# Performance work log

Hardware: AMD Instinct MI355X
Metric: run time of the kernel (lower is better)

The kernel has to match this reference:

```python
import jax, jax.numpy as jnp
import numpy as np

B, S, IN_DIM, D_MODEL, H = 8, 1024, 512, 1024, 16
DEPTH = D_MODEL // H
LN_EPS = 1e-5


def setup_inputs() -> dict:
    key = jax.random.key(0)
    ks = jax.random.split(key, 10)
    def xavier(k, shape):
        fan_in, fan_out = shape[0], shape[1]
        lim = float(np.sqrt(6.0 / (fan_in + fan_out)))
        return jax.random.uniform(k, shape, jnp.float32, -lim, lim)
    return {
        "x": jax.random.normal(ks[0], (B, S, IN_DIM), jnp.float32),
        "mask": jax.random.randint(ks[1], (H, S, S), 0, 2, jnp.int32),
        "wq_w": xavier(ks[2], (IN_DIM, D_MODEL)),
        "wq_b": jnp.zeros((D_MODEL,), jnp.float32),
        "wk_w": xavier(ks[3], (IN_DIM, D_MODEL)),
        "wk_b": jnp.zeros((D_MODEL,), jnp.float32),
        "wv_w": xavier(ks[4], (IN_DIM, D_MODEL)),
        "wv_b": jnp.zeros((D_MODEL,), jnp.float32),
        "dense_w": xavier(ks[5], (D_MODEL, D_MODEL)),
        "dense_b": jnp.zeros((D_MODEL,), jnp.float32),
        "res_w": xavier(ks[6], (IN_DIM, D_MODEL)),  # residual_linear (no bias)
        "ln_g": 1.0 + 0.02 * jax.random.normal(ks[7], (D_MODEL,), jnp.float32),
        "ln_b": 0.02 * jax.random.normal(ks[8], (D_MODEL,), jnp.float32),
    }


def reference(x, mask, wq_w, wq_b, wk_w, wk_b, wv_w, wv_b,
              dense_w, dense_b, res_w, ln_g, ln_b):
    bs = x.shape[0]
    residual = x @ res_w  # [B,S,D_MODEL]
    # project and split heads -> [B,H,S,depth]
    def split(t):
        return t.reshape(bs, -1, H, DEPTH).transpose(0, 2, 1, 3)
    q = split(x @ wq_w + wq_b)
    k = split(x @ wk_w + wk_b)
    v = split(x @ wv_w + wv_b)
    scale = 1.0 / jnp.sqrt(jnp.asarray(DEPTH, x.dtype))
    attn = jnp.einsum("bhqd,bhkd->bhqk", q, k) * scale
    attn = jnp.where(mask[None] == 0, jnp.asarray(-1e9, attn.dtype), attn)
    attn = jax.nn.softmax(attn, axis=-1)  # dropout is identity in eval
    out = jnp.einsum("bhqk,bhkd->bhqd", attn, v)
    out = out.transpose(0, 2, 1, 3).reshape(bs, -1, D_MODEL)
    out = out @ dense_w + dense_b
    # residual + LayerNorm
    y = residual + out
    mu = jnp.mean(y, axis=-1, keepdims=True)
    var = jnp.mean(jnp.square(y - mu), axis=-1, keepdims=True)
    y = (y - mu) * jax.lax.rsqrt(var + LN_EPS)
    return y * ln_g + ln_b
```

## Files before the change

kernel.cpp:

```cpp
#include <hip/hip_runtime.h>
#include <stdint.h>

#define B_ 8
#define S_ 1024
#define IN_DIM 512
#define DM 1024
#define H_ 16
#define DEP 64

typedef __bf16 bf16;
typedef __attribute__((ext_vector_type(8))) __bf16 bf16x8;
typedef __attribute__((ext_vector_type(4))) __bf16 bf16x4;
typedef __attribute__((ext_vector_type(4))) float f32x4;

static __device__ __forceinline__ void gld_lds16(const void* g, void* l) {
    __builtin_amdgcn_global_load_lds(
        (const __attribute__((address_space(1))) uint32_t*)g,
        (__attribute__((address_space(3))) uint32_t*)l, 16, 0, 0);
}

__global__ void detect_kernel(const uint16_t* __restrict__ xraw, int* __restrict__ flag) {
    const int t = threadIdx.x;
    int sane = 0;
    #pragma unroll
    for (int j = 0; j < 8; j++) {
        const uint16_t u = xraw[t * 8 + j];
        const int e = (u >> 7) & 0xff;
        sane += ((u & 0x7fff) == 0 || (e >= 100 && e <= 140)) ? 1 : 0;
    }
    #pragma unroll
    for (int m = 1; m < 64; m <<= 1) sane += __shfl_xor(sane, m);
    if (t == 0) *flag = (sane >= 450) ? 1 : 0;
}

static __device__ __forceinline__ float ldin(const void* p, size_t i, int isb) {
    return isb ? (float)((const bf16*)p)[i] : ((const float*)p)[i];
}

__global__ __launch_bounds__(256) void transpose_kernel(
    const void* __restrict__ wq, const void* __restrict__ wk, const void* __restrict__ wv,
    const void* __restrict__ res, const void* __restrict__ dense,
    bf16* __restrict__ wqT, bf16* __restrict__ wkT, bf16* __restrict__ wvT,
    bf16* __restrict__ resT, bf16* __restrict__ denseT, const int* __restrict__ flag)
{
    const int isb = *flag;
    __shared__ bf16 tile[32][33];
    const int z = blockIdx.z;
    const void* src; bf16* dst; int kb, kd;
    if (z == 0)      { src = wq;    dst = wqT;    kb = 0;   kd = 512;  }
    else if (z == 1) { src = wk;    dst = wkT;    kb = 0;   kd = 512;  }
    else if (z == 2) { src = wv;    dst = wvT;    kb = 0;   kd = 512;  }
    else if (z == 3) { src = res;   dst = resT;   kb = 0;   kd = 512;  }
    else if (z == 4) { src = dense; dst = denseT; kb = 0;   kd = 1024; }
    else             { src = dense; dst = denseT; kb = 512; kd = 1024; }
    const int n0 = blockIdx.x * 32, k0 = blockIdx.y * 32;
    const int tx = threadIdx.x, ty = threadIdx.y;
    #pragma unroll
    for (int r = 0; r < 4; r++)
        tile[ty + r*8][tx] = (bf16)ldin(src, (size_t)(kb + k0 + ty + r*8) * DM + n0 + tx, isb);
    __syncthreads();
    #pragma unroll
    for (int r = 0; r < 4; r++)
        dst[(size_t)(n0 + ty + r*8) * kd + kb + k0 + tx] = tile[tx][ty + r*8];
}

__global__ __launch_bounds__(256) void xconv_kernel(
    const void* __restrict__ x, bf16* __restrict__ xc, const int* __restrict__ flag)
{
    const int isb = *flag;
    const size_t i = ((size_t)blockIdx.x * 256 + threadIdx.x) * 4;
    #pragma unroll
    for (int j = 0; j < 4; j++) xc[i + j] = (bf16)ldin(x, i + j, isb);
}

__global__ __launch_bounds__(256) void smallconv_kernel(
    const void* b0, const void* b1, const void* b2, const void* b3,
    const void* b4, const void* b5, bf16* __restrict__ out, const int* __restrict__ flag)
{
    const int isb = *flag;
    const void* srcs[6] = {b0, b1, b2, b3, b4, b5};
    const void* s = srcs[blockIdx.x];
    for (int i = threadIdx.x; i < 1024; i += 256)
        out[blockIdx.x * 1024 + i] = (bf16)ldin(s, i, isb);
}

__global__ __launch_bounds__(256) void maskpack_kernel(
    const int* __restrict__ mask, unsigned long long* __restrict__ mb)
{
    const int w = threadIdx.x >> 6, lane = threadIdx.x & 63;
    const int gw = blockIdx.x * 4 + w;
    for (int c = gw; c < 262144; c += 4096) {
        const int v = mask[(size_t)c * 64 + lane];
        const unsigned long long bits = __ballot(v != 0);
        if (lane == 0) mb[c] = bits;
    }
}

template<int KDIM>
static __device__ __forceinline__ void gemm_core(
    const bf16* __restrict__ A, const bf16* __restrict__ BT,
    int m0, int n0, bf16* Asm, bf16* Bsm, f32x4 acc[4][4])
{
    const int tid = threadIdx.x, l = tid & 63, w = tid >> 6;
    const int wm = w >> 1, wn = w & 1, quad = l >> 4, l15 = l & 15;
    #pragma unroll
    for (int i = 0; i < 4; i++)
        #pragma unroll
        for (int j = 0; j < 4; j++) acc[i][j] = f32x4{0.f, 0.f, 0.f, 0.f};

    for (int k0 = 0; k0 < KDIM; k0 += 32) {
        __syncthreads();
        #pragma unroll
        for (int qq = 0; qq < 2; qq++) {
            const int c = qq*256 + tid;
            const int row = c >> 2, ch = c & 3;
            gld_lds16(A  + (size_t)(m0 + row)*KDIM + k0 + ch*8, Asm + (qq*256 + w*64)*8);
            gld_lds16(BT + (size_t)(n0 + row)*KDIM + k0 + ch*8, Bsm + (qq*256 + w*64)*8);
        }
        __syncthreads();
        bf16x8 af[4], bfv[4];
        #pragma unroll
        for (int i = 0; i < 4; i++)
            af[i] = *(const bf16x8*)(Asm + (wm*64 + i*16 + l15)*32 + quad*8);
        #pragma unroll
        for (int j = 0; j < 4; j++)
            bfv[j] = *(const bf16x8*)(Bsm + (wn*64 + j*16 + l15)*32 + quad*8);
        #pragma unroll
        for (int i = 0; i < 4; i++)
            #pragma unroll
            for (int j = 0; j < 4; j++)
                acc[i][j] = __builtin_amdgcn_mfma_f32_16x16x32_bf16(af[i], bfv[j], acc[i][j], 0, 0, 0);
    }
}

#define EPI_P 132
__global__ __launch_bounds__(256) void proj_kernel(
    const bf16* __restrict__ x,
    const bf16* __restrict__ wqT, const bf16* __restrict__ wkT,
    const bf16* __restrict__ wvT, const bf16* __restrict__ resT,
    const bf16* __restrict__ small,
    bf16* __restrict__ Q, bf16* __restrict__ K, bf16* __restrict__ VtG, bf16* __restrict__ R)
{
    __shared__ alignas(16) char smem[17408];
    bf16* Asm = (bf16*)smem;
    bf16* Bsm = (bf16*)(smem + 8192);
    bf16* epi = (bf16*)smem;

    const int m0 = blockIdx.x * 128;
    const int ng = blockIdx.y * 128;
    const int sel = ng >> 10, n0 = ng & 1023;
    const bf16* BT; const bf16* bias = nullptr;
    if (sel == 0)      { BT = wqT; bias = small;        }
    else if (sel == 1) { BT = wkT; bias = small + 1024; }
    else if (sel == 2) { BT = wvT; bias = small + 2048; }
    else               { BT = resT; }

    f32x4 acc[4][4];
    gemm_core<IN_DIM>(x, BT, m0, n0, Asm, Bsm, acc);

    const int tid = threadIdx.x, l = tid & 63, w = tid >> 6;
    const int wm = w >> 1, wn = w & 1, quad = l >> 4, l15 = l & 15;

    if (sel == 2) {
        const int bb = m0 >> 10, srow0 = m0 & 1023;
        #pragma unroll
        for (int hf = 0; hf < 2; hf++) {
            __syncthreads();
            if (wn == hf) {
                #pragma unroll
                for (int j = 0; j < 4; j++) {
                    const int cl = j*16 + l15;
                    const float bv = (float)bias[n0 + hf*64 + cl];
                    #pragma unroll
                    for (int i = 0; i < 4; i++) {
                        const int rho = wm*64 + i*16 + quad*4;
                        #pragma unroll
                        for (int r = 0; r < 4; r++)
                            epi[cl*EPI_P + rho + r] = (bf16)(acc[i][j][r] + bv);
                    }
                }
            }
            __syncthreads();
            const int hh = (n0 >> 6) + hf;
            const int sc = tid & 15;
            #pragma unroll
            for (int pass = 0; pass < 4; pass++) {
                const int dl = (tid >> 4) + pass*16;
                bf16x8 v;
                #pragma unroll
                for (int k = 0; k < 8; k++) v[k] = epi[dl*EPI_P + sc*8 + k];
                *(bf16x8*)(VtG + ((size_t)(bb*16 + hh)*64 + dl)*S_ + srow0 + sc*8) = v;
            }
        }
        return;
    }

    #pragma unroll
    for (int j = 0; j < 4; j++) {
        const int col = n0 + wn*64 + j*16 + l15;
        const float bv = (sel < 3) ? (float)bias[col] : 0.f;
        #pragma unroll
        for (int i = 0; i < 4; i++) {
            const int rb = m0 + wm*64 + i*16 + quad*4;
            #pragma unroll
            for (int r = 0; r < 4; r++) {
                const float v = acc[i][j][r] + bv;
                if (sel == 0)      Q[(size_t)(rb + r)*DM + col] = (bf16)(v * 0.125f);
                else if (sel == 1) K[(size_t)(rb + r)*DM + col] = (bf16)v;
                else               R[(size_t)(rb + r)*DM + col] = (bf16)v;
            }
        }
    }
}

#define KP 68
__global__ __launch_bounds__(256) void attn_kernel(
    const bf16* __restrict__ Q, const bf16* __restrict__ K, const bf16* __restrict__ VtG,
    const unsigned long long* __restrict__ mb, bf16* __restrict__ AO)
{
    __shared__ alignas(16) bf16 Ksm[64*KP];
    __shared__ alignas(16) bf16 Vsm[64*KP];
    __shared__ alignas(16) bf16 Psm[4*16*40];

    const int tid = threadIdx.x, l = tid & 63, w = tid >> 6;
    const int quad = l >> 4, l15 = l & 15;
    const int b = blockIdx.y >> 4, h = blockIdx.y & 15;
    const int wrow = blockIdx.x*128 + w*32;
    const size_t rowbase = (size_t)b * S_;
    bf16* pp = Psm + w*640;

    bf16x8 qa[2][2];
    #pragma unroll
    for (int g = 0; g < 2; g++) {
        const bf16* qp = Q + (rowbase + wrow + g*16 + l15)*DM + h*DEP + quad*8;
        qa[g][0] = *(const bf16x8*)qp;
        qa[g][1] = *(const bf16x8*)(qp + 32);
    }
    const bf16* kgbase = K + rowbase*DM + h*DEP;
    const bf16* vgbase = VtG + (size_t)(b*16 + h)*64*S_;
    const unsigned long long* mrow[2][4];
    #pragma unroll
    for (int g = 0; g < 2; g++)
        #pragma unroll
        for (int r = 0; r < 4; r++)
            mrow[g][r] = mb + ((size_t)h*S_ + wrow + g*16 + quad*4 + r) * 16;

    f32x4 o[2][4];
    float lsum[2][4];
    #pragma unroll
    for (int g = 0; g < 2; g++)
        #pragma unroll
        for (int dt = 0; dt < 4; dt++) { o[g][dt] = f32x4{0.f,0.f,0.f,0.f}; lsum[g][dt] = 0.f; }

    const int srow = tid >> 3, sch = tid & 7;

    for (int kt = 0; kt < S_; kt += 64) {
        uint32_t mw[2][2][4];
        #pragma unroll
        for (int g = 0; g < 2; g++)
            #pragma unroll
            for (int r = 0; r < 4; r++) {
                const unsigned long long m = mrow[g][r][kt >> 6];
                mw[g][0][r] = (uint32_t)m;
                mw[g][1][r] = (uint32_t)(m >> 32);
            }
        const bf16x8 k0v = *(const bf16x8*)(kgbase + (size_t)(kt + srow)*DM + sch*8);
        const bf16x8 k1v = *(const bf16x8*)(kgbase + (size_t)(kt + 32 + srow)*DM + sch*8);
        const bf16x8 v0v = *(const bf16x8*)(vgbase + (size_t)srow*S_ + kt + sch*8);
        const bf16x8 v1v = *(const bf16x8*)(vgbase + (size_t)(32 + srow)*S_ + kt + sch*8);
        __syncthreads();
        *(bf16x8*)(Ksm + srow*KP + sch*8)        = k0v;
        *(bf16x8*)(Ksm + (32 + srow)*KP + sch*8) = k1v;
        *(bf16x8*)(Vsm + srow*KP + sch*8)        = v0v;
        *(bf16x8*)(Vsm + (32 + srow)*KP + sch*8) = v1v;
        __syncthreads();

        #pragma unroll
        for (int sub = 0; sub < 2; sub++) {
            bf16x8 kf[2][2], vf[4];
            #pragma unroll
            for (int h2 = 0; h2 < 2; h2++) {
                const bf16* kp = Ksm + (sub*32 + h2*16 + l15)*KP + quad*8;
                kf[h2][0] = *(const bf16x8*)kp;
                kf[h2][1] = *(const bf16x8*)(kp + 32);
            }
            #pragma unroll
            for (int dt = 0; dt < 4; dt++)
                vf[dt] = *(const bf16x8*)(Vsm + (dt*16 + l15)*KP + sub*32 + quad*8);

            #pragma unroll
            for (int g = 0; g < 2; g++) {
                f32x4 s2[2];
                #pragma unroll
                for (int h2 = 0; h2 < 2; h2++) {
                    f32x4 z = {0.f,0.f,0.f,0.f};
                    z = __builtin_amdgcn_mfma_f32_16x16x32_bf16(qa[g][0], kf[h2][0], z, 0, 0, 0);
                    z = __builtin_amdgcn_mfma_f32_16x16x32_bf16(qa[g][1], kf[h2][1], z, 0, 0, 0);
                    s2[h2] = z;
                }
                float p[2][4];
                #pragma unroll
                for (int h2 = 0; h2 < 2; h2++)
                    #pragma unroll
                    for (int r = 0; r < 4; r++) {
                        const float e = __expf(s2[h2][r]);
                        p[h2][r] = ((mw[g][sub][r] >> (h2*16 + l15)) & 1u) ? e : 0.f;
                    }
                #pragma unroll
                for (int r = 0; r < 4; r++) lsum[g][r] += p[0][r] + p[1][r];
                #pragma unroll
                for (int h2 = 0; h2 < 2; h2++)
                    #pragma unroll
                    for (int r = 0; r < 4; r++)
                        pp[(quad*4 + r)*40 + h2*16 + l15] = (bf16)p[h2][r];
                __asm__ volatile("s_waitcnt lgkmcnt(0)" ::: "memory");
                const bf16x8 pa = *(const bf16x8*)(pp + l15*40 + quad*8);
                #pragma unroll
                for (int dt = 0; dt < 4; dt++)
                    o[g][dt] = __builtin_amdgcn_mfma_f32_16x16x32_bf16(pa, vf[dt], o[g][dt], 0, 0, 0);
            }
        }
    }

    #pragma unroll
    for (int g = 0; g < 2; g++)
        #pragma unroll
        for (int r = 0; r < 4; r++) {
            float t = lsum[g][r];
            t += __shfl_xor(t, 1); t += __shfl_xor(t, 2);
            t += __shfl_xor(t, 4); t += __shfl_xor(t, 8);
            const float inv = 1.0f / t;
            #pragma unroll
            for (int dt = 0; dt < 4; dt++)
                AO[(rowbase + wrow + g*16 + quad*4 + r)*DM + h*DEP + dt*16 + l15] =
                    (bf16)(o[g][dt][r] * inv);
        }
}

__global__ __launch_bounds__(256) void dense_kernel(
    const bf16* __restrict__ AOin, const bf16* __restrict__ dT,
    const bf16* __restrict__ db, bf16* __restrict__ R)
{
    __shared__ alignas(16) bf16 Asm[128*32];
    __shared__ alignas(16) bf16 Bsm[128*32];
    const int m0 = blockIdx.x * 128, n0 = blockIdx.y * 128;
    f32x4 acc[4][4];
    gemm_core<DM>(AOin, dT, m0, n0, Asm, Bsm, acc);
    const int tid = threadIdx.x, l = tid & 63, w = tid >> 6;
    const int wm = w >> 1, wn = w & 1, quad = l >> 4, l15 = l & 15;
    #pragma unroll
    for (int j = 0; j < 4; j++) {
        const int col = n0 + wn*64 + j*16 + l15;
        const float bv = (float)db[col];
        #pragma unroll
        for (int i = 0; i < 4; i++) {
            const int rb = m0 + wm*64 + i*16 + quad*4;
            #pragma unroll
            for (int r = 0; r < 4; r++) {
                const size_t idx = (size_t)(rb + r)*DM + col;
                R[idx] = (bf16)((float)R[idx] + acc[i][j][r] + bv);
            }
        }
    }
}

__global__ __launch_bounds__(256) void ln_kernel(
    const bf16* __restrict__ R, const bf16* __restrict__ small,
    void* __restrict__ out, const int* __restrict__ flag)
{
    const int isb = *flag;
    __shared__ float red[8];
    const int row = blockIdx.x, tid = threadIdx.x;
    const bf16x4 rv = *(const bf16x4*)(R + (size_t)row*DM + tid*4);
    const float vx = (float)rv[0], vy = (float)rv[1], vz = (float)rv[2], vw = (float)rv[3];
    float s = vx + vy + vz + vw;
    #pragma unroll
    for (int m = 1; m < 64; m <<= 1) s += __shfl_xor(s, m);
    const int w = tid >> 6;
    if ((tid & 63) == 0) red[w] = s;
    __syncthreads();
    const float mu = (red[0] + red[1] + red[2] + red[3]) * (1.0f/DM);
    const float dx = vx - mu, dy = vy - mu, dz = vz - mu, dw = vw - mu;
    float q = dx*dx + dy*dy + dz*dz + dw*dw;
    #pragma unroll
    for (int m = 1; m < 64; m <<= 1) q += __shfl_xor(q, m);
    if ((tid & 63) == 0) red[4 + w] = q;
    __syncthreads();
    const float var = (red[4] + red[5] + red[6] + red[7]) * (1.0f/DM);
    const float rstd = rsqrtf(var + 1e-5f);
    const int col = tid * 4;
    const bf16x4 gv = *(const bf16x4*)(small + 4*1024 + col);
    const bf16x4 bv = *(const bf16x4*)(small + 5*1024 + col);
    const float o0 = dx*rstd*(float)gv[0] + (float)bv[0];
    const float o1 = dy*rstd*(float)gv[1] + (float)bv[1];
    const float o2 = dz*rstd*(float)gv[2] + (float)bv[2];
    const float o3 = dw*rstd*(float)gv[3] + (float)bv[3];
    if (isb) {
        bf16x4 ov; ov[0] = (bf16)o0; ov[1] = (bf16)o1; ov[2] = (bf16)o2; ov[3] = (bf16)o3;
        *(bf16x4*)((bf16*)out + (size_t)row*DM + col) = ov;
    } else {
        float4 ov = {o0, o1, o2, o3};
        *(float4*)((float*)out + (size_t)row*DM + col) = ov;
    }
}

extern "C" void kernel_launch(void* const* d_in, const int* in_sizes, int n_in,
                              void* d_out, int out_size, void* d_ws, size_t ws_size,
                              hipStream_t stream) {
    const int* mask = (const int*)d_in[1];

    char* ws = (char*)d_ws;
    bf16* wqT   = (bf16*)(ws);
    bf16* wkT   = (bf16*)(ws + ((size_t)1 << 20));
    bf16* wvT   = (bf16*)(ws + ((size_t)2 << 20));
    bf16* resT  = (bf16*)(ws + ((size_t)3 << 20));
    bf16* dT    = (bf16*)(ws + ((size_t)4 << 20));
    bf16* small = (bf16*)(ws + ((size_t)6 << 20));
    int*  flag  = (int*) (ws + ((size_t)6 << 20) + 16384);
    unsigned long long* mbits = (unsigned long long*)(ws + ((size_t)7 << 20));
    bf16* Qb    = (bf16*)(ws + ((size_t)9  << 20));
    bf16* Kb    = (bf16*)(ws + ((size_t)25 << 20));
    bf16* VtG   = (bf16*)(ws + ((size_t)41 << 20));
    bf16* R     = (bf16*)(ws + ((size_t)57 << 20));
    bf16* xc    = (bf16*)d_out;

    detect_kernel<<<1, 64, 0, stream>>>((const uint16_t*)d_in[0], flag);
    transpose_kernel<<<dim3(32, 16, 6), dim3(32, 8), 0, stream>>>(
        d_in[2], d_in[4], d_in[6], d_in[10], d_in[8],
        wqT, wkT, wvT, resT, dT, flag);
    xconv_kernel<<<4096, 256, 0, stream>>>(d_in[0], xc, flag);
    smallconv_kernel<<<6, 256, 0, stream>>>(
        d_in[3], d_in[5], d_in[7], d_in[9], d_in[11], d_in[12], small, flag);
    maskpack_kernel<<<1024, 256, 0, stream>>>(mask, mbits);
    proj_kernel<<<dim3(64, 32), 256, 0, stream>>>(
        xc, wqT, wkT, wvT, resT, small, Qb, Kb, VtG, R);
    attn_kernel<<<dim3(8, 128), 256, 0, stream>>>(Qb, Kb, VtG, mbits, Qb );
    dense_kernel<<<dim3(64, 8), 256, 0, stream>>>(Qb, dT, small + 3*1024, R);
    ln_kernel<<<8192, 256, 0, stream>>>(R, small, d_out, flag);
}
```

Measured before the change: 391.0 us.

## Prefetch K/V tiles into registers and pass P through shuffles instead of LDS

```diff
diff --git a/kernel.cpp b/kernel.cpp
--- a/kernel.cpp
+++ b/kernel.cpp
@@ -214,20 +214,25 @@
 }
 
 #define KP 68
+
+static __device__ __forceinline__ uint32_t pk2(float a, float b) {
+    union { bf16 h[2]; uint32_t u; } c;
+    c.h[0] = (bf16)a; c.h[1] = (bf16)b;
+    return c.u;
+}
+
 __global__ __launch_bounds__(256) void attn_kernel(
     const bf16* __restrict__ Q, const bf16* __restrict__ K, const bf16* __restrict__ VtG,
     const unsigned long long* __restrict__ mb, bf16* __restrict__ AO)
 {
     __shared__ alignas(16) bf16 Ksm[64*KP];
     __shared__ alignas(16) bf16 Vsm[64*KP];
-    __shared__ alignas(16) bf16 Psm[4*16*40];
 
     const int tid = threadIdx.x, l = tid & 63, w = tid >> 6;
     const int quad = l >> 4, l15 = l & 15;
     const int b = blockIdx.y >> 4, h = blockIdx.y & 15;
     const int wrow = blockIdx.x*128 + w*32;
     const size_t rowbase = (size_t)b * S_;
-    bf16* pp = Psm + w*640;
 
     bf16x8 qa[2][2];
     #pragma unroll
@@ -238,36 +243,36 @@
     }
     const bf16* kgbase = K + rowbase*DM + h*DEP;
     const bf16* vgbase = VtG + (size_t)(b*16 + h)*64*S_;
-    const unsigned long long* mrow[2][4];
+    const unsigned long long* mbase[2];
     #pragma unroll
     for (int g = 0; g < 2; g++)
-        #pragma unroll
-        for (int r = 0; r < 4; r++)
-            mrow[g][r] = mb + ((size_t)h*S_ + wrow + g*16 + quad*4 + r) * 16;
+        mbase[g] = mb + ((size_t)h*S_ + wrow + g*16 + l15) * 16;
 
     f32x4 o[2][4];
-    float lsum[2][4];
+    float lsum[2] = {0.f, 0.f};
     #pragma unroll
     for (int g = 0; g < 2; g++)
         #pragma unroll
-        for (int dt = 0; dt < 4; dt++) { o[g][dt] = f32x4{0.f,0.f,0.f,0.f}; lsum[g][dt] = 0.f; }
+        for (int dt = 0; dt < 4; dt++) o[g][dt] = f32x4{0.f,0.f,0.f,0.f};
 
     const int srow = tid >> 3, sch = tid & 7;
 
-    for (int kt = 0; kt < S_; kt += 64) {
-        uint32_t mw[2][2][4];
-        #pragma unroll
-        for (int g = 0; g < 2; g++)
-            #pragma unroll
-            for (int r = 0; r < 4; r++) {
-                const unsigned long long m = mrow[g][r][kt >> 6];
-                mw[g][0][r] = (uint32_t)m;
-                mw[g][1][r] = (uint32_t)(m >> 32);
-            }
-        const bf16x8 k0v = *(const bf16x8*)(kgbase + (size_t)(kt + srow)*DM + sch*8);
-        const bf16x8 k1v = *(const bf16x8*)(kgbase + (size_t)(kt + 32 + srow)*DM + sch*8);
-        const bf16x8 v0v = *(const bf16x8*)(vgbase + (size_t)srow*S_ + kt + sch*8);
-        const bf16x8 v1v = *(const bf16x8*)(vgbase + (size_t)(32 + srow)*S_ + kt + sch*8);
+    bf16x8 k0v = *(const bf16x8*)(kgbase + (size_t)srow*DM + sch*8);
+    bf16x8 k1v = *(const bf16x8*)(kgbase + (size_t)(32 + srow)*DM + sch*8);
+    bf16x8 v0v = *(const bf16x8*)(vgbase + (size_t)srow*S_ + sch*8);
+    bf16x8 v1v = *(const bf16x8*)(vgbase + (size_t)(32 + srow)*S_ + sch*8);
+    uint32_t mlo[2], mhi[2];
+    #pragma unroll
+    for (int g = 0; g < 2; g++) {
+        const unsigned long long mword = mbase[g][0];
+        mlo[g] = (uint32_t)mword; mhi[g] = (uint32_t)(mword >> 32);
+    }
+
+    const int srcA = ((quad & 1) << 5) + l15;
+    const int srcB = srcA + 16;
+    const bool hiq = quad >= 2;
+
+    for (int it = 0; it < 16; it++) {
         __syncthreads();
         *(bf16x8*)(Ksm + srow*KP + sch*8)        = k0v;
         *(bf16x8*)(Ksm + (32 + srow)*KP + sch*8) = k1v;
@@ -275,6 +280,20 @@
         *(bf16x8*)(Vsm + (32 + srow)*KP + sch*8) = v1v;
         __syncthreads();
 
+        const uint32_t cmlo[2] = {mlo[0], mlo[1]}, cmhi[2] = {mhi[0], mhi[1]};
+        if (it + 1 < 16) {
+            const int nkt = (it + 1) * 64;
+            k0v = *(const bf16x8*)(kgbase + (size_t)(nkt + srow)*DM + sch*8);
+            k1v = *(const bf16x8*)(kgbase + (size_t)(nkt + 32 + srow)*DM + sch*8);
+            v0v = *(const bf16x8*)(vgbase + (size_t)srow*S_ + nkt + sch*8);
+            v1v = *(const bf16x8*)(vgbase + (size_t)(32 + srow)*S_ + nkt + sch*8);
+            #pragma unroll
+            for (int g = 0; g < 2; g++) {
+                const unsigned long long mword = mbase[g][it + 1];
+                mlo[g] = (uint32_t)mword; mhi[g] = (uint32_t)(mword >> 32);
+            }
+        }
+
         #pragma unroll
         for (int sub = 0; sub < 2; sub++) {
             bf16x8 kf[2][2], vf[4];
@@ -290,46 +309,54 @@
 
             #pragma unroll
             for (int g = 0; g < 2; g++) {
-                f32x4 s2[2];
+                f32x4 st[2];
                 #pragma unroll
                 for (int h2 = 0; h2 < 2; h2++) {
                     f32x4 z = {0.f,0.f,0.f,0.f};
-                    z = __builtin_amdgcn_mfma_f32_16x16x32_bf16(qa[g][0], kf[h2][0], z, 0, 0, 0);
-                    z = __builtin_amdgcn_mfma_f32_16x16x32_bf16(qa[g][1], kf[h2][1], z, 0, 0, 0);
-                    s2[h2] = z;
+                    z = __builtin_amdgcn_mfma_f32_16x16x32_bf16(kf[h2][0], qa[g][0], z, 0, 0, 0);
+                    z = __builtin_amdgcn_mfma_f32_16x16x32_bf16(kf[h2][1], qa[g][1], z, 0, 0, 0);
+                    st[h2] = z;
                 }
+                const uint32_t msk = sub ? cmhi[g] : cmlo[g];
                 float p[2][4];
                 #pragma unroll
-                for (int h2 = 0; h2 < 2; h2++)
+                for (int h2 = 0; h2 < 2; h2++) {
+                    const uint32_t nib = (msk >> (h2*16 + quad*4)) & 0xfu;
                     #pragma unroll
                     for (int r = 0; r < 4; r++) {
-                        const float e = __expf(s2[h2][r]);
-                        p[h2][r] = ((mw[g][sub][r] >> (h2*16 + l15)) & 1u) ? e : 0.f;
+                        const float e = __expf(st[h2][r]);
+                        p[h2][r] = ((nib >> r) & 1u) ? e : 0.f;
                     }
-                #pragma unroll
-                for (int r = 0; r < 4; r++) lsum[g][r] += p[0][r] + p[1][r];
-                #pragma unroll
-                for (int h2 = 0; h2 < 2; h2++)
-                    #pragma unroll
-                    for (int r = 0; r < 4; r++)
-                        pp[(quad*4 + r)*40 + h2*16 + l15] = (bf16)p[h2][r];
-                __asm__ volatile("s_waitcnt lgkmcnt(0)" ::: "memory");
-                const bf16x8 pa = *(const bf16x8*)(pp + l15*40 + quad*8);
+                }
+                lsum[g] += (p[0][0]+p[0][1]+p[0][2]+p[0][3]) + (p[1][0]+p[1][1]+p[1][2]+p[1][3]);
+                const uint32_t pk00 = pk2(p[0][0], p[0][1]), pk01 = pk2(p[0][2], p[0][3]);
+                const uint32_t pk10 = pk2(p[1][0], p[1][1]), pk11 = pk2(p[1][2], p[1][3]);
+                const int d0a = __shfl((int)pk00, srcA), d0b = __shfl((int)pk10, srcA);
+                const int d1a = __shfl((int)pk01, srcA), d1b = __shfl((int)pk11, srcA);
+                const int d2a = __shfl((int)pk00, srcB), d2b = __shfl((int)pk10, srcB);
+                const int d3a = __shfl((int)pk01, srcB), d3b = __shfl((int)pk11, srcB);
+                union { uint32_t u[4]; bf16x8 v; } pa;
+                pa.u[0] = (uint32_t)(hiq ? d0b : d0a);
+                pa.u[1] = (uint32_t)(hiq ? d1b : d1a);
+                pa.u[2] = (uint32_t)(hiq ? d2b : d2a);
+                pa.u[3] = (uint32_t)(hiq ? d3b : d3a);
                 #pragma unroll
                 for (int dt = 0; dt < 4; dt++)
-                    o[g][dt] = __builtin_amdgcn_mfma_f32_16x16x32_bf16(pa, vf[dt], o[g][dt], 0, 0, 0);
-            }
-        }
-    }
-
+                    o[g][dt] = __builtin_amdgcn_mfma_f32_16x16x32_bf16(pa.v, vf[dt], o[g][dt], 0, 0, 0);
+            }
+        }
+    }
+
+    #pragma unroll
+    for (int g = 0; g < 2; g++) {
+        lsum[g] += __shfl_xor(lsum[g], 16);
+        lsum[g] += __shfl_xor(lsum[g], 32);
+    }
     #pragma unroll
     for (int g = 0; g < 2; g++)
         #pragma unroll
         for (int r = 0; r < 4; r++) {
-            float t = lsum[g][r];
-            t += __shfl_xor(t, 1); t += __shfl_xor(t, 2);
-            t += __shfl_xor(t, 4); t += __shfl_xor(t, 8);
-            const float inv = 1.0f / t;
+            const float inv = 1.0f / __shfl(lsum[g], quad*4 + r);
             #pragma unroll
             for (int dt = 0; dt < 4; dt++)
                 AO[(rowbase + wrow + g*16 + quad*4 + r)*DM + h*DEP + dt*16 + l15] =
```

Result: no change. 396.2 us (+1.3%).
